# Kernel tuning notes

Hardware: AMD Instinct MI355X
Metric: run time of the kernel (lower is better)

## Reference

```python
import jax, jax.numpy as jnp
import numpy as np


def _grid_sample_3d(vol, pts):
    """Trilinear grid_sample, align_corners=True, padding_mode='border'.
    vol: [C, D, H, W]; pts: [N, 3] with (x, y, z) in normalized [-1, 1] coords
    (x indexes W, y indexes H, z indexes D, matching torch.grid_sample).
    Returns [N, C]."""
    C, D, H, W = vol.shape
    def to_idx(c, size):
        c = (c + 1.0) * 0.5 * (size - 1)
        return jnp.clip(c, 0.0, size - 1.0)  # border padding
    ix = to_idx(pts[:, 0], W)
    iy = to_idx(pts[:, 1], H)
    iz = to_idx(pts[:, 2], D)
    x0 = jnp.floor(ix); y0 = jnp.floor(iy); z0 = jnp.floor(iz)
    wx = ix - x0;       wy = iy - y0;       wz = iz - z0
    x0i = x0.astype(jnp.int32); x1i = jnp.minimum(x0i + 1, W - 1)
    y0i = y0.astype(jnp.int32); y1i = jnp.minimum(y0i + 1, H - 1)
    z0i = z0.astype(jnp.int32); z1i = jnp.minimum(z0i + 1, D - 1)
    g = lambda zi, yi, xi: vol[:, zi, yi, xi]  # [C, N]
    out = (g(z0i, y0i, x0i) * (1 - wz) * (1 - wy) * (1 - wx)
         + g(z0i, y0i, x1i) * (1 - wz) * (1 - wy) * wx
         + g(z0i, y1i, x0i) * (1 - wz) * wy * (1 - wx)
         + g(z0i, y1i, x1i) * (1 - wz) * wy * wx
         + g(z1i, y0i, x0i) * wz * (1 - wy) * (1 - wx)
         + g(z1i, y0i, x1i) * wz * (1 - wy) * wx
         + g(z1i, y1i, x0i) * wz * wy * (1 - wx)
         + g(z1i, y1i, x1i) * wz * wy * wx)
    return out.T  # [N, C]


def _skinning(x, w, tfs):
    """x: [B,N,3], w: [B,N,J], tfs: [B,J,4,4] -> (xd [B,N,3], w_tf [B,N,4,4])."""
    x_h = jnp.concatenate([x, jnp.ones_like(x[..., :1])], axis=-1)  # [B,N,4]
    w_tf = jnp.einsum('bpn,bnij->bpij', w, tfs)                      # [B,N,4,4]
    xh = jnp.einsum('bpij,bpj->bpi', w_tf, x_h)                      # [B,N,4]
    return xh[..., :3], w_tf


def setup_inputs() -> dict:
    key = jax.random.key(0)
    ks = jax.random.split(key, 12)
    B, N, J = 4, 250000, 55
    return {
        'xc': jax.random.normal(ks[0], (B, N, 3), jnp.float32),
        'shape_offset': jax.random.normal(ks[1], (B, N, 3), jnp.float32),
        'pose_offset': jax.random.normal(ks[2], (B, N, 3), jnp.float32),
        'tfs': jax.random.normal(ks[3], (B, J, 4, 4), jnp.float32),
        'tfs_inv': jax.random.normal(ks[4], (1, J, 4, 4), jnp.float32),
        'poseoff_ori': jax.random.normal(ks[5], (1, N, 3), jnp.float32),
        'lbsw': jax.random.uniform(ks[6], (1, N, J), jnp.float32),
        'mask': jax.random.randint(ks[7], (1, N), 0, 2).astype(bool),
        'lbs_voxel': jax.random.uniform(ks[8], (1, J, 16, 64, 64), jnp.float32),
        'offset_kernel': jnp.zeros((1, 1, 3), jnp.float32),
        'scale_kernel': jax.random.uniform(ks[9], (1, 1, 3), jnp.float32),
    }


def reference(xc, shape_offset, pose_offset, tfs, tfs_inv, poseoff_ori,
              lbsw, mask, lbs_voxel, offset_kernel, scale_kernel):
    B = xc.shape[0]
    # query_weights: normalize then trilinear grid sample of shared voxel
    xn = (xc + offset_kernel) * scale_kernel  # [B,N,3]
    vol = lbs_voxel[0]                        # [J,16,64,64], shared across batch
    w = jax.vmap(lambda p: _grid_sample_3d(vol, p))(xn)  # [B,N,J]
    # w[:, mask[0]] = lbsw[mask]
    w = jnp.where(mask[0][None, :, None], lbsw, w)
    # first blend: canonical with tfs_inv (inverse=False path)
    xc_cano, w_tf_inv = _skinning(xc, w, jnp.broadcast_to(tfs_inv, (B,) + tfs_inv.shape[1:]))
    xc_cano_ori = xc_cano - poseoff_ori
    xc_shape = xc_cano_ori + shape_offset + pose_offset
    # second blend: posed with tfs
    xd, w_tf = _skinning(xc_shape, w, tfs)
    w_tf_all = w_tf @ w_tf_inv  # [B,N,4,4] batched 4x4 matmul
    return xd, w_tf_all
```

## Files before the change

### kernel.cpp

```cpp
#include <hip/hip_runtime.h>


#define JNT 55
#define VD  16
#define VH  64
#define VW  64
#define NVOX (VD * VH * VW)

__global__ __launch_bounds__(256, 1) void build_mats_k(
    const float* __restrict__ vol,
    const float* __restrict__ tfs,
    const float* __restrict__ tfs_inv,
    float* __restrict__ Mi_tab,
    float* __restrict__ Mv_tab,
    int B)
{
    int v = blockIdx.x * blockDim.x + threadIdx.x;
    if (v >= NVOX) return;
    float w[JNT];
#pragma unroll
    for (int j = 0; j < JNT; ++j) w[j] = vol[j * NVOX + v];

    float M[16];
#pragma unroll
    for (int i = 0; i < 16; ++i) M[i] = 0.f;
#pragma unroll
    for (int j = 0; j < JNT; ++j) {
        float wj = w[j];
#pragma unroll
        for (int i = 0; i < 16; ++i) M[i] = fmaf(wj, tfs_inv[j * 16 + i], M[i]);
    }
    float4* dst = (float4*)(Mi_tab + (size_t)v * 16);
#pragma unroll
    for (int g = 0; g < 4; ++g)
        dst[g] = make_float4(M[4*g+0], M[4*g+1], M[4*g+2], M[4*g+3]);

    for (int b = 0; b < B; ++b) {
        const float* tb = tfs + (size_t)b * JNT * 16;
#pragma unroll
        for (int i = 0; i < 16; ++i) M[i] = 0.f;
#pragma unroll
        for (int j = 0; j < JNT; ++j) {
            float wj = w[j];
#pragma unroll
            for (int i = 0; i < 16; ++i) M[i] = fmaf(wj, tb[j * 16 + i], M[i]);
        }
        float4* dv = (float4*)(Mv_tab + ((size_t)b * NVOX + v) * 16);
#pragma unroll
        for (int g = 0; g < 4; ++g)
            dv[g] = make_float4(M[4*g+0], M[4*g+1], M[4*g+2], M[4*g+3]);
    }
}

template <bool USE_TAB>
__global__ __launch_bounds__(256, 4) void deformer_k(
    const float* __restrict__ xc,
    const float* __restrict__ shape_off,
    const float* __restrict__ pose_off,
    const float* __restrict__ tfs,
    const float* __restrict__ tfs_inv,
    const float* __restrict__ poseoff_ori,
    const float* __restrict__ lbsw,
    const int*   __restrict__ mask,
    const float* __restrict__ vol,
    const float* __restrict__ Mi_tab,
    const float* __restrict__ Mv_tab,
    const float* __restrict__ offk,
    const float* __restrict__ sck,
    float* __restrict__ out_xd,
    float* __restrict__ out_w,
    int N)
{
    int n = blockIdx.x * blockDim.x + threadIdx.x;
    int b = blockIdx.y;
    if (n >= N) return;
    size_t pid = (size_t)b * N + n;
    size_t p3  = pid * 3;

    float x = xc[p3 + 0], y = xc[p3 + 1], z = xc[p3 + 2];

    float A[16], Ai[16];
#pragma unroll
    for (int i = 0; i < 16; ++i) { A[i] = 0.f; Ai[i] = 0.f; }

    bool m = (mask[n] != 0);
    if (m) {
        const float* lp = lbsw + (size_t)n * JNT;
        const float* tb = tfs + (size_t)b * JNT * 16;
#pragma unroll
        for (int j = 0; j < JNT; ++j) {
            float wj = lp[j];
#pragma unroll
            for (int i = 0; i < 16; ++i) Ai[i] = fmaf(wj, tfs_inv[j * 16 + i], Ai[i]);
#pragma unroll
            for (int i = 0; i < 16; ++i) A[i]  = fmaf(wj, tb[j * 16 + i],      A[i]);
        }
    } else {
        float px = (x + offk[0]) * sck[0];
        float py = (y + offk[1]) * sck[1];
        float pz = (z + offk[2]) * sck[2];
        float ix = fminf(fmaxf((px + 1.f) * 0.5f * (VW - 1), 0.f), (float)(VW - 1));
        float iy = fminf(fmaxf((py + 1.f) * 0.5f * (VH - 1), 0.f), (float)(VH - 1));
        float iz = fminf(fmaxf((pz + 1.f) * 0.5f * (VD - 1), 0.f), (float)(VD - 1));
        float fx = floorf(ix), fy = floorf(iy), fz = floorf(iz);
        float wx = ix - fx,    wy = iy - fy,    wz = iz - fz;
        int x0 = (int)fx, y0 = (int)fy, z0 = (int)fz;
        int x1 = min(x0 + 1, VW - 1);
        int y1 = min(y0 + 1, VH - 1);
        int z1 = min(z0 + 1, VD - 1);

        if (USE_TAB) {
            float cwx[2] = {1.f - wx, wx};
            float cwy[2] = {1.f - wy, wy};
            float cwz[2] = {1.f - wz, wz};
            int   xs[2] = {x0, x1}, ys[2] = {y0, y1}, zs[2] = {z0, z1};
            const float* Mvb = Mv_tab + (size_t)b * NVOX * 16;
#pragma unroll
            for (int cz = 0; cz < 2; ++cz)
#pragma unroll
            for (int cy = 0; cy < 2; ++cy)
#pragma unroll
            for (int cx = 0; cx < 2; ++cx) {
                float cw = cwz[cz] * cwy[cy] * cwx[cx];
                size_t vox = (size_t)(zs[cz] * VH + ys[cy]) * VW + xs[cx];
                const float4* pi = (const float4*)(Mi_tab + vox * 16);
                const float4* pv = (const float4*)(Mvb    + vox * 16);
#pragma unroll
                for (int g = 0; g < 4; ++g) {
                    float4 mi = pi[g];
                    Ai[4*g+0] = fmaf(cw, mi.x, Ai[4*g+0]);
                    Ai[4*g+1] = fmaf(cw, mi.y, Ai[4*g+1]);
                    Ai[4*g+2] = fmaf(cw, mi.z, Ai[4*g+2]);
                    Ai[4*g+3] = fmaf(cw, mi.w, Ai[4*g+3]);
                }
#pragma unroll
                for (int g = 0; g < 4; ++g) {
                    float4 mv = pv[g];
                    A[4*g+0] = fmaf(cw, mv.x, A[4*g+0]);
                    A[4*g+1] = fmaf(cw, mv.y, A[4*g+1]);
                    A[4*g+2] = fmaf(cw, mv.z, A[4*g+2]);
                    A[4*g+3] = fmaf(cw, mv.w, A[4*g+3]);
                }
            }
        } else {
            float w00 = (1.f - wz) * (1.f - wy), w01 = (1.f - wz) * wy;
            float w10 = wz * (1.f - wy),         w11 = wz * wy;
            int o00 = (z0 * VH + y0) * VW, o01 = (z0 * VH + y1) * VW;
            int o10 = (z1 * VH + y0) * VW, o11 = (z1 * VH + y1) * VW;
            const float* tb = tfs + (size_t)b * JNT * 16;
#pragma unroll
            for (int j = 0; j < JNT; ++j) {
                const float* vp = vol + (size_t)j * NVOX;
                float v000 = vp[o00 + x0], v001 = vp[o00 + x1];
                float v010 = vp[o01 + x0], v011 = vp[o01 + x1];
                float v100 = vp[o10 + x0], v101 = vp[o10 + x1];
                float v110 = vp[o11 + x0], v111 = vp[o11 + x1];
                float c0 = w00 * v000 + w01 * v010 + w10 * v100 + w11 * v110;
                float c1 = w00 * v001 + w01 * v011 + w10 * v101 + w11 * v111;
                float wj = c0 + wx * (c1 - c0);
#pragma unroll
                for (int i = 0; i < 16; ++i) Ai[i] = fmaf(wj, tfs_inv[j*16+i], Ai[i]);
#pragma unroll
                for (int i = 0; i < 16; ++i) A[i]  = fmaf(wj, tb[j*16+i],      A[i]);
            }
        }
    }

    float c0 = Ai[0]*x + Ai[1]*y + Ai[2]*z  + Ai[3];
    float c1 = Ai[4]*x + Ai[5]*y + Ai[6]*z  + Ai[7];
    float c2 = Ai[8]*x + Ai[9]*y + Ai[10]*z + Ai[11];
    size_t n3 = (size_t)n * 3;
    float sx = c0 - poseoff_ori[n3 + 0] + shape_off[p3 + 0] + pose_off[p3 + 0];
    float sy = c1 - poseoff_ori[n3 + 1] + shape_off[p3 + 1] + pose_off[p3 + 1];
    float sz = c2 - poseoff_ori[n3 + 2] + shape_off[p3 + 2] + pose_off[p3 + 2];
    float d0 = A[0]*sx + A[1]*sy + A[2]*sz  + A[3];
    float d1 = A[4]*sx + A[5]*sy + A[6]*sz  + A[7];
    float d2 = A[8]*sx + A[9]*sy + A[10]*sz + A[11];
    out_xd[p3 + 0] = d0;
    out_xd[p3 + 1] = d1;
    out_xd[p3 + 2] = d2;

    float4* ow = (float4*)(out_w + pid * 16);
#pragma unroll
    for (int i = 0; i < 4; ++i) {
        float a0 = A[i*4+0], a1 = A[i*4+1], a2 = A[i*4+2], a3 = A[i*4+3];
        float4 r;
        r.x = a0*Ai[0] + a1*Ai[4] + a2*Ai[8]  + a3*Ai[12];
        r.y = a0*Ai[1] + a1*Ai[5] + a2*Ai[9]  + a3*Ai[13];
        r.z = a0*Ai[2] + a1*Ai[6] + a2*Ai[10] + a3*Ai[14];
        r.w = a0*Ai[3] + a1*Ai[7] + a2*Ai[11] + a3*Ai[15];
        ow[i] = r;
    }
}

extern "C" void kernel_launch(void* const* d_in, const int* in_sizes, int n_in,
                              void* d_out, int out_size, void* d_ws, size_t ws_size,
                              hipStream_t stream)
{
    const float* xc    = (const float*)d_in[0];
    const float* shoff = (const float*)d_in[1];
    const float* pooff = (const float*)d_in[2];
    const float* tfs   = (const float*)d_in[3];
    const float* tfsi  = (const float*)d_in[4];
    const float* poori = (const float*)d_in[5];
    const float* lbsw  = (const float*)d_in[6];
    const int*   mask  = (const int*)d_in[7];
    const float* vol   = (const float*)d_in[8];
    const float* offk  = (const float*)d_in[9];
    const float* sck   = (const float*)d_in[10];

    int N = in_sizes[5] / 3;
    int B = in_sizes[0] / (3 * N);
    float* out_xd = (float*)d_out;
    float* out_w  = (float*)d_out + (size_t)B * N * 3;

    size_t tbytes = (size_t)NVOX * 16 * (1 + B) * sizeof(float);
    float* Mi_tab = (float*)d_ws;
    float* Mv_tab = Mi_tab + (size_t)NVOX * 16;
    bool use_tab = (ws_size >= tbytes);

    dim3 blk(256);
    dim3 grd((N + 255) / 256, B);

    if (use_tab) {
        build_mats_k<<<dim3((NVOX + 255) / 256), blk, 0, stream>>>(
            vol, tfs, tfsi, Mi_tab, Mv_tab, B);
        deformer_k<true><<<grd, blk, 0, stream>>>(
            xc, shoff, pooff, tfs, tfsi, poori, lbsw, mask, vol, Mi_tab, Mv_tab,
            offk, sck, out_xd, out_w, N);
    } else {
        deformer_k<false><<<grd, blk, 0, stream>>>(
            xc, shoff, pooff, tfs, tfsi, poori, lbsw, mask, vol, Mi_tab, Mv_tab,
            offk, sck, out_xd, out_w, N);
    }
}
```

Measured before the change: 335.3 us.

## Store per-voxel blend matrices in fp16 interleaved table and compact masked/unmasked points

The precomputed per-voxel skinning matrices are stored as fp16 with the inverse and forward matrices interleaved per batch, which halves table traffic and gives each corner one 64-byte contiguous read. Inside each block, masked and unmasked points are compacted with ballot and prefix counts so that whole wavefronts take one path, removing divergence between the lbsw path and the grid-sample path. Corner loads are double-buffered. In exchange, the inverse matrix is duplicated per batch, fp16 rounding lowers matrix precision, and the compaction adds shared-memory bookkeeping and barriers.

```diff
diff --git a/kernel.cpp b/kernel.cpp
--- a/kernel.cpp
+++ b/kernel.cpp
@@ -1,4 +1,5 @@
 #include <hip/hip_runtime.h>
+#include <hip/hip_fp16.h>
 
 
 #define JNT 55
@@ -7,95 +8,184 @@
 #define VW  64
 #define NVOX (VD * VH * VW)
 
-__global__ __launch_bounds__(256, 1) void build_mats_k(
-    const float* __restrict__ vol,
+__global__ __launch_bounds__(256, 2) void build_tab_k(
+    const float* __restrict__ vol, const float* __restrict__ tfs,
+    const float* __restrict__ tfs_inv, __half* __restrict__ tab, int B)
+{
+    int v = blockIdx.x * 256 + threadIdx.x;
+    if (v >= NVOX) return;
+    float w[JNT];
+#pragma unroll
+    for (int j = 0; j < JNT; ++j) w[j] = vol[j * NVOX + v];
+
+    float Mi[16];
+#pragma unroll
+    for (int i = 0; i < 16; ++i) Mi[i] = 0.f;
+#pragma unroll
+    for (int j = 0; j < JNT; ++j) {
+        float wj = w[j];
+#pragma unroll
+        for (int i = 0; i < 16; ++i) Mi[i] = fmaf(wj, tfs_inv[j * 16 + i], Mi[i]);
+    }
+    float hi[8];
+#pragma unroll
+    for (int i = 0; i < 8; ++i)
+        hi[i] = __builtin_bit_cast(float, __floats2half2_rn(Mi[2*i], Mi[2*i+1]));
+
+    for (int b = 0; b < B; ++b) {
+        const float* tb = tfs + (size_t)b * JNT * 16;
+        float Mv[16];
+#pragma unroll
+        for (int i = 0; i < 16; ++i) Mv[i] = 0.f;
+#pragma unroll
+        for (int j = 0; j < JNT; ++j) {
+            float wj = w[j];
+#pragma unroll
+            for (int i = 0; i < 16; ++i) Mv[i] = fmaf(wj, tb[j * 16 + i], Mv[i]);
+        }
+        float hv[8];
+#pragma unroll
+        for (int i = 0; i < 8; ++i)
+            hv[i] = __builtin_bit_cast(float, __floats2half2_rn(Mv[2*i], Mv[2*i+1]));
+
+        float4* d4 = (float4*)(tab + ((size_t)b * NVOX + v) * 32);
+        d4[0] = make_float4(hi[0], hi[1], hi[2], hi[3]);
+        d4[1] = make_float4(hi[4], hi[5], hi[6], hi[7]);
+        d4[2] = make_float4(hv[0], hv[1], hv[2], hv[3]);
+        d4[3] = make_float4(hv[4], hv[5], hv[6], hv[7]);
+    }
+}
+
+__device__ __forceinline__ void acc8(float cw, float4 r, float* a)
+{
+    float rr[4] = {r.x, r.y, r.z, r.w};
+#pragma unroll
+    for (int k = 0; k < 4; ++k) {
+        __half2 h = __builtin_bit_cast(__half2, rr[k]);
+        float2 f = __half22float2(h);
+        a[2*k]     = fmaf(cw, f.x, a[2*k]);
+        a[2*k + 1] = fmaf(cw, f.y, a[2*k + 1]);
+    }
+}
+
+__device__ __forceinline__ void epilogue(
+    int b, int n, int N, float x, float y, float z,
+    const float* A, const float* Ai,
+    const float* __restrict__ shoff, const float* __restrict__ pooff,
+    const float* __restrict__ poori,
+    float* __restrict__ out_xd, float* __restrict__ out_w)
+{
+    size_t pid = (size_t)b * N + n;
+    size_t p3  = pid * 3;
+    size_t n3  = (size_t)n * 3;
+    float c0 = Ai[0]*x + Ai[1]*y + Ai[2]*z  + Ai[3];
+    float c1 = Ai[4]*x + Ai[5]*y + Ai[6]*z  + Ai[7];
+    float c2 = Ai[8]*x + Ai[9]*y + Ai[10]*z + Ai[11];
+    float sx = c0 - poori[n3 + 0] + shoff[p3 + 0] + pooff[p3 + 0];
+    float sy = c1 - poori[n3 + 1] + shoff[p3 + 1] + pooff[p3 + 1];
+    float sz = c2 - poori[n3 + 2] + shoff[p3 + 2] + pooff[p3 + 2];
+    out_xd[p3 + 0] = A[0]*sx + A[1]*sy + A[2]*sz  + A[3];
+    out_xd[p3 + 1] = A[4]*sx + A[5]*sy + A[6]*sz  + A[7];
+    out_xd[p3 + 2] = A[8]*sx + A[9]*sy + A[10]*sz + A[11];
+
+    float4* ow = (float4*)(out_w + pid * 16);
+#pragma unroll
+    for (int i = 0; i < 4; ++i) {
+        float a0 = A[i*4+0], a1 = A[i*4+1], a2 = A[i*4+2], a3 = A[i*4+3];
+        float4 r;
+        r.x = a0*Ai[0] + a1*Ai[4] + a2*Ai[8]  + a3*Ai[12];
+        r.y = a0*Ai[1] + a1*Ai[5] + a2*Ai[9]  + a3*Ai[13];
+        r.z = a0*Ai[2] + a1*Ai[6] + a2*Ai[10] + a3*Ai[14];
+        r.w = a0*Ai[3] + a1*Ai[7] + a2*Ai[11] + a3*Ai[15];
+        ow[i] = r;
+    }
+}
+
+template <bool USE_TAB>
+__global__ __launch_bounds__(256, 3) void deform_k(
+    const float* __restrict__ xc,
+    const float* __restrict__ shoff,
+    const float* __restrict__ pooff,
     const float* __restrict__ tfs,
     const float* __restrict__ tfs_inv,
-    float* __restrict__ Mi_tab,
-    float* __restrict__ Mv_tab,
-    int B)
-{
-    int v = blockIdx.x * blockDim.x + threadIdx.x;
-    if (v >= NVOX) return;
-    float w[JNT];
-#pragma unroll
-    for (int j = 0; j < JNT; ++j) w[j] = vol[j * NVOX + v];
-
-    float M[16];
-#pragma unroll
-    for (int i = 0; i < 16; ++i) M[i] = 0.f;
-#pragma unroll
-    for (int j = 0; j < JNT; ++j) {
-        float wj = w[j];
-#pragma unroll
-        for (int i = 0; i < 16; ++i) M[i] = fmaf(wj, tfs_inv[j * 16 + i], M[i]);
-    }
-    float4* dst = (float4*)(Mi_tab + (size_t)v * 16);
-#pragma unroll
-    for (int g = 0; g < 4; ++g)
-        dst[g] = make_float4(M[4*g+0], M[4*g+1], M[4*g+2], M[4*g+3]);
-
-    for (int b = 0; b < B; ++b) {
-        const float* tb = tfs + (size_t)b * JNT * 16;
-#pragma unroll
-        for (int i = 0; i < 16; ++i) M[i] = 0.f;
-#pragma unroll
-        for (int j = 0; j < JNT; ++j) {
-            float wj = w[j];
-#pragma unroll
-            for (int i = 0; i < 16; ++i) M[i] = fmaf(wj, tb[j * 16 + i], M[i]);
-        }
-        float4* dv = (float4*)(Mv_tab + ((size_t)b * NVOX + v) * 16);
-#pragma unroll
-        for (int g = 0; g < 4; ++g)
-            dv[g] = make_float4(M[4*g+0], M[4*g+1], M[4*g+2], M[4*g+3]);
-    }
-}
-
-template <bool USE_TAB>
-__global__ __launch_bounds__(256, 4) void deformer_k(
-    const float* __restrict__ xc,
-    const float* __restrict__ shape_off,
-    const float* __restrict__ pose_off,
-    const float* __restrict__ tfs,
-    const float* __restrict__ tfs_inv,
-    const float* __restrict__ poseoff_ori,
+    const float* __restrict__ poori,
     const float* __restrict__ lbsw,
     const int*   __restrict__ mask,
+    const __half* __restrict__ tab,
     const float* __restrict__ vol,
-    const float* __restrict__ Mi_tab,
-    const float* __restrict__ Mv_tab,
     const float* __restrict__ offk,
     const float* __restrict__ sck,
     float* __restrict__ out_xd,
     float* __restrict__ out_w,
     int N)
 {
-    int n = blockIdx.x * blockDim.x + threadIdx.x;
-    int b = blockIdx.y;
-    if (n >= N) return;
-    size_t pid = (size_t)b * N + n;
-    size_t p3  = pid * 3;
-
-    float x = xc[p3 + 0], y = xc[p3 + 1], z = xc[p3 + 2];
-
-    float A[16], Ai[16];
-#pragma unroll
-    for (int i = 0; i < 16; ++i) { A[i] = 0.f; Ai[i] = 0.f; }
-
-    bool m = (mask[n] != 0);
-    if (m) {
-        const float* lp = lbsw + (size_t)n * JNT;
-        const float* tb = tfs + (size_t)b * JNT * 16;
-#pragma unroll
+    int b    = blockIdx.y;
+    int base = blockIdx.x * 256;
+    int tx   = threadIdx.x;
+    int nc   = base + tx;
+    bool valid = nc < N;
+    bool m = valid && (mask[nc] != 0);
+
+    __shared__ unsigned short ml[256], ul[256];
+    __shared__ int sc[10];
+
+    int lane = tx & 63, wid = tx >> 6;
+    unsigned long long bm = __ballot(m);
+    unsigned long long bu = __ballot(valid && !m);
+    if (lane == 0) { sc[wid] = (int)__popcll(bm); sc[4 + wid] = (int)__popcll(bu); }
+    __syncthreads();
+    if (tx == 0) {
+        int s = 0;
+        for (int i = 0; i < 4; ++i) { int t = sc[i]; sc[i] = s; s += t; }
+        sc[8] = s; s = 0;
+        for (int i = 0; i < 4; ++i) { int t = sc[4 + i]; sc[4 + i] = s; s += t; }
+        sc[9] = s;
+    }
+    __syncthreads();
+    unsigned long long below = ((unsigned long long)1 << lane) - 1;
+    if (m)          ml[sc[wid]     + (int)__popcll(bm & below)] = (unsigned short)tx;
+    else if (valid) ul[sc[4 + wid] + (int)__popcll(bu & below)] = (unsigned short)tx;
+    __syncthreads();
+    int mcnt = sc[8], ucnt = sc[9];
+
+    if (tx < mcnt) {
+        int n = base + ml[tx];
+        size_t p3 = ((size_t)b * N + n) * 3;
+        float x = xc[p3], y = xc[p3 + 1], z = xc[p3 + 2];
+        float A[16], Ai[16];
+#pragma unroll
+        for (int i = 0; i < 16; ++i) { A[i] = 0.f; Ai[i] = 0.f; }
+        const float*  lp  = lbsw + (size_t)n * JNT;
+        const float4* ti4 = (const float4*)tfs_inv;
+        const float4* tb4 = (const float4*)(tfs + (size_t)b * JNT * 16);
         for (int j = 0; j < JNT; ++j) {
             float wj = lp[j];
 #pragma unroll
-            for (int i = 0; i < 16; ++i) Ai[i] = fmaf(wj, tfs_inv[j * 16 + i], Ai[i]);
-#pragma unroll
-            for (int i = 0; i < 16; ++i) A[i]  = fmaf(wj, tb[j * 16 + i],      A[i]);
+            for (int q = 0; q < 4; ++q) {
+                float4 r = ti4[j * 4 + q];
+                Ai[4*q+0] = fmaf(wj, r.x, Ai[4*q+0]);
+                Ai[4*q+1] = fmaf(wj, r.y, Ai[4*q+1]);
+                Ai[4*q+2] = fmaf(wj, r.z, Ai[4*q+2]);
+                Ai[4*q+3] = fmaf(wj, r.w, Ai[4*q+3]);
+            }
+#pragma unroll
+            for (int q = 0; q < 4; ++q) {
+                float4 r = tb4[j * 4 + q];
+                A[4*q+0] = fmaf(wj, r.x, A[4*q+0]);
+                A[4*q+1] = fmaf(wj, r.y, A[4*q+1]);
+                A[4*q+2] = fmaf(wj, r.z, A[4*q+2]);
+                A[4*q+3] = fmaf(wj, r.w, A[4*q+3]);
+            }
         }
-    } else {
+        epilogue(b, n, N, x, y, z, A, Ai, shoff, pooff, poori, out_xd, out_w);
+    }
+
+    int ub = 255 - tx;
+    if (ub < ucnt) {
+        int n = base + ul[ub];
+        size_t p3 = ((size_t)b * N + n) * 3;
+        float x = xc[p3], y = xc[p3 + 1], z = xc[p3 + 2];
+
         float px = (x + offk[0]) * sck[0];
         float py = (y + offk[1]) * sck[1];
         float pz = (z + offk[2]) * sck[2];
@@ -109,37 +199,41 @@
         int y1 = min(y0 + 1, VH - 1);
         int z1 = min(z0 + 1, VD - 1);
 
+        float A[16], Ai[16];
+#pragma unroll
+        for (int i = 0; i < 16; ++i) { A[i] = 0.f; Ai[i] = 0.f; }
+
         if (USE_TAB) {
             float cwx[2] = {1.f - wx, wx};
             float cwy[2] = {1.f - wy, wy};
             float cwz[2] = {1.f - wz, wz};
             int   xs[2] = {x0, x1}, ys[2] = {y0, y1}, zs[2] = {z0, z1};
-            const float* Mvb = Mv_tab + (size_t)b * NVOX * 16;
-#pragma unroll
-            for (int cz = 0; cz < 2; ++cz)
-#pragma unroll
-            for (int cy = 0; cy < 2; ++cy)
-#pragma unroll
-            for (int cx = 0; cx < 2; ++cx) {
-                float cw = cwz[cz] * cwy[cy] * cwx[cx];
-                size_t vox = (size_t)(zs[cz] * VH + ys[cy]) * VW + xs[cx];
-                const float4* pi = (const float4*)(Mi_tab + vox * 16);
-                const float4* pv = (const float4*)(Mvb    + vox * 16);
-#pragma unroll
-                for (int g = 0; g < 4; ++g) {
-                    float4 mi = pi[g];
-                    Ai[4*g+0] = fmaf(cw, mi.x, Ai[4*g+0]);
-                    Ai[4*g+1] = fmaf(cw, mi.y, Ai[4*g+1]);
-                    Ai[4*g+2] = fmaf(cw, mi.z, Ai[4*g+2]);
-                    Ai[4*g+3] = fmaf(cw, mi.w, Ai[4*g+3]);
-                }
-#pragma unroll
-                for (int g = 0; g < 4; ++g) {
-                    float4 mv = pv[g];
-                    A[4*g+0] = fmaf(cw, mv.x, A[4*g+0]);
-                    A[4*g+1] = fmaf(cw, mv.y, A[4*g+1]);
-                    A[4*g+2] = fmaf(cw, mv.z, A[4*g+2]);
-                    A[4*g+3] = fmaf(cw, mv.w, A[4*g+3]);
+            int   vox[8]; float cw[8];
+#pragma unroll
+            for (int c = 0; c < 8; ++c) {
+                int cz = c >> 2, cy = (c >> 1) & 1, cx = c & 1;
+                vox[c] = (zs[cz] * VH + ys[cy]) * VW + xs[cx];
+                cw[c]  = cwz[cz] * cwy[cy] * cwx[cx];
+            }
+            const __half* tbb = tab + (size_t)b * NVOX * 32;
+            float4 s0[4], s1[4];
+            {
+                const float4* p0 = (const float4*)(tbb + (size_t)vox[0] * 32);
+                const float4* p1 = (const float4*)(tbb + (size_t)vox[1] * 32);
+                s0[0]=p0[0]; s0[1]=p0[1]; s0[2]=p0[2]; s0[3]=p0[3];
+                s1[0]=p1[0]; s1[1]=p1[1]; s1[2]=p1[2]; s1[3]=p1[3];
+            }
+#pragma unroll
+            for (int c = 0; c < 8; ++c) {
+                float4* cur = (c & 1) ? s1 : s0;
+                float cwc = cw[c];
+                acc8(cwc, cur[0], Ai);
+                acc8(cwc, cur[1], Ai + 8);
+                acc8(cwc, cur[2], A);
+                acc8(cwc, cur[3], A + 8);
+                if (c + 2 < 8) {
+                    const float4* pn = (const float4*)(tbb + (size_t)vox[c + 2] * 32);
+                    cur[0]=pn[0]; cur[1]=pn[1]; cur[2]=pn[2]; cur[3]=pn[3];
                 }
             }
         } else {
@@ -148,7 +242,7 @@
             int o00 = (z0 * VH + y0) * VW, o01 = (z0 * VH + y1) * VW;
             int o10 = (z1 * VH + y0) * VW, o11 = (z1 * VH + y1) * VW;
             const float* tb = tfs + (size_t)b * JNT * 16;
-#pragma unroll
+#pragma unroll 4
             for (int j = 0; j < JNT; ++j) {
                 const float* vp = vol + (size_t)j * NVOX;
                 float v000 = vp[o00 + x0], v001 = vp[o00 + x1];
@@ -164,32 +258,7 @@
                 for (int i = 0; i < 16; ++i) A[i]  = fmaf(wj, tb[j*16+i],      A[i]);
             }
         }
-    }
-
-    float c0 = Ai[0]*x + Ai[1]*y + Ai[2]*z  + Ai[3];
-    float c1 = Ai[4]*x + Ai[5]*y + Ai[6]*z  + Ai[7];
-    float c2 = Ai[8]*x + Ai[9]*y + Ai[10]*z + Ai[11];
-    size_t n3 = (size_t)n * 3;
-    float sx = c0 - poseoff_ori[n3 + 0] + shape_off[p3 + 0] + pose_off[p3 + 0];
-    float sy = c1 - poseoff_ori[n3 + 1] + shape_off[p3 + 1] + pose_off[p3 + 1];
-    float sz = c2 - poseoff_ori[n3 + 2] + shape_off[p3 + 2] + pose_off[p3 + 2];
-    float d0 = A[0]*sx + A[1]*sy + A[2]*sz  + A[3];
-    float d1 = A[4]*sx + A[5]*sy + A[6]*sz  + A[7];
-    float d2 = A[8]*sx + A[9]*sy + A[10]*sz + A[11];
-    out_xd[p3 + 0] = d0;
-    out_xd[p3 + 1] = d1;
-    out_xd[p3 + 2] = d2;
-
-    float4* ow = (float4*)(out_w + pid * 16);
-#pragma unroll
-    for (int i = 0; i < 4; ++i) {
-        float a0 = A[i*4+0], a1 = A[i*4+1], a2 = A[i*4+2], a3 = A[i*4+3];
-        float4 r;
-        r.x = a0*Ai[0] + a1*Ai[4] + a2*Ai[8]  + a3*Ai[12];
-        r.y = a0*Ai[1] + a1*Ai[5] + a2*Ai[9]  + a3*Ai[13];
-        r.z = a0*Ai[2] + a1*Ai[6] + a2*Ai[10] + a3*Ai[14];
-        r.w = a0*Ai[3] + a1*Ai[7] + a2*Ai[11] + a3*Ai[15];
-        ow[i] = r;
+        epilogue(b, n, N, x, y, z, A, Ai, shoff, pooff, poori, out_xd, out_w);
     }
 }
 
@@ -214,23 +283,21 @@
     float* out_xd = (float*)d_out;
     float* out_w  = (float*)d_out + (size_t)B * N * 3;
 
-    size_t tbytes = (size_t)NVOX * 16 * (1 + B) * sizeof(float);
-    float* Mi_tab = (float*)d_ws;
-    float* Mv_tab = Mi_tab + (size_t)NVOX * 16;
+    size_t tbytes = (size_t)B * NVOX * 32 * sizeof(__half);
+    __half* tab = (__half*)d_ws;
     bool use_tab = (ws_size >= tbytes);
 
     dim3 blk(256);
     dim3 grd((N + 255) / 256, B);
 
     if (use_tab) {
-        build_mats_k<<<dim3((NVOX + 255) / 256), blk, 0, stream>>>(
-            vol, tfs, tfsi, Mi_tab, Mv_tab, B);
-        deformer_k<true><<<grd, blk, 0, stream>>>(
-            xc, shoff, pooff, tfs, tfsi, poori, lbsw, mask, vol, Mi_tab, Mv_tab,
-            offk, sck, out_xd, out_w, N);
+        build_tab_k<<<dim3((NVOX + 255) / 256), blk, 0, stream>>>(vol, tfs, tfsi, tab, B);
+        deform_k<true><<<grd, blk, 0, stream>>>(
+            xc, shoff, pooff, tfs, tfsi, poori, lbsw, mask, tab, vol, offk, sck,
+            out_xd, out_w, N);
     } else {
-        deformer_k<false><<<grd, blk, 0, stream>>>(
-            xc, shoff, pooff, tfs, tfsi, poori, lbsw, mask, vol, Mi_tab, Mv_tab,
-            offk, sck, out_xd, out_w, N);
-    }
-}
+        deform_k<false><<<grd, blk, 0, stream>>>(
+            xc, shoff, pooff, tfs, tfsi, poori, lbsw, mask, tab, vol, offk, sck,
+            out_xd, out_w, N);
+    }
+}
```

Result: slower. 408.6 us (+21.9%).
